# Performance work log

Measured on AMD Instinct MI355X. Metric: run time of the kernel, lower is better.

The kernel has to match this reference:

```python
import jax, jax.numpy as jnp
import numpy as np

DIM = 1024

def _circ_conv(x, key):
    # circular convolution along last dim via FFT
    D = x.shape[-1]
    return jnp.fft.irfft(jnp.fft.rfft(x, axis=-1) * jnp.fft.rfft(key), n=D, axis=-1)

def _circ_corr(x, key):
    # circular correlation: conjugate the key spectrum
    D = x.shape[-1]
    return jnp.fft.irfft(jnp.fft.rfft(x, axis=-1) * jnp.conj(jnp.fft.rfft(key)), n=D, axis=-1)

def setup_inputs() -> dict:
    key = jax.random.key(0)
    k0, k1, k2 = jax.random.split(key, 3)
    B, T, D = 4, 2048, DIM
    x = jax.random.normal(k0, (B, T, D), dtype=jnp.float32)
    bind_key = jax.random.normal(k1, (D,), dtype=jnp.float32) * 0.02
    unbind_key = jax.random.normal(k2, (D,), dtype=jnp.float32) * 0.02
    gate = jnp.ones((1,), dtype=jnp.float32)
    decay = jnp.asarray(0.9, dtype=jnp.float32)
    return {"x": x, "bind_key": bind_key, "unbind_key": unbind_key, "gate": gate, "decay": decay}

def reference(x, bind_key, unbind_key, gate, decay):
    B, T, D = x.shape
    bound = _circ_conv(x, bind_key)                      # (B, T, D)
    d = jax.nn.sigmoid(decay)
    pos = jnp.arange(T, dtype=x.dtype)
    diff = pos[:, None] - pos[None, :]                   # (T, T)
    causal = diff >= 0
    # clamp exponent to avoid inf*0 on masked (t < s) entries; math identical to tril mask
    decay_matrix = jnp.where(causal, d ** jnp.maximum(diff, 0.0), 0.0)
    hologram = jnp.einsum('ts,bsd->btd', decay_matrix, bound)
    retrieved = _circ_corr(hologram, unbind_key)
    return x + gate * retrieved
```

## Files before the change

kernel.cpp:

```cpp
#include <hip/hip_runtime.h>
#include <hip/hip_bf16.h>

constexpr int Dd = 1024;
constexpr int Tt = 2048;
constexpr int Bb = 4;
constexpr int Rr = Bb * Tt;
constexpr int NCH = 32;
constexpr int CL  = 64;
constexpr int HOR = 32;
constexpr int SCB = Bb * NCH * 2;
constexpr int CBL = 64;
constexpr int RSN = 1032;

typedef __attribute__((ext_vector_type(2))) float f32x2;
typedef __attribute__((ext_vector_type(4))) float f32x4;
typedef __attribute__((ext_vector_type(16))) float f32x16;
typedef __attribute__((ext_vector_type(8))) short bf16x8;

__device__ __forceinline__ float sigmoidf_(float v) {
    return 1.0f / (1.0f + expf(-v));
}

__device__ __forceinline__ short bf16bits(float f) {
    union { __hip_bfloat16 b; short s; } u;
    u.b = __float2bfloat16(f);
    return u.s;
}

__device__ __forceinline__ void async16(const void* g, void* l) {
    __builtin_amdgcn_global_load_lds(
        (const __attribute__((address_space(1))) unsigned int*)g,
        (__attribute__((address_space(3))) unsigned int*)l,
        16, 0, 0);
}

__global__ void k_scan(const float* __restrict__ x,
                       const float* __restrict__ bind,
                       const float* __restrict__ unbind,
                       const float* __restrict__ decay,
                       __hip_bfloat16* __restrict__ xs,
                       float* __restrict__ c) {
    __shared__ float sb[Dd];
    __shared__ float su[Dd];
    __shared__ float sp[256];

    const int tid = threadIdx.x;
    if (blockIdx.x >= CBL) {
        const int sid = blockIdx.x - CBL;
        const int dh = sid & 1;
        const int ch = (sid >> 1) & (NCH - 1);
        const int b  = sid >> 6;
        const float dd = sigmoidf_(decay[0]);
        const int t0 = ch * CL;
        const int d  = dh * 512 + tid * 2;
        f32x2 h = (f32x2){0.f, 0.f};
        if (ch != 0) {
            const size_t pb = ((size_t)b * Tt + (size_t)(t0 - HOR)) * Dd + d;
            #pragma unroll 8
            for (int t = 0; t < HOR; ++t) {
                f32x2 v = *(const f32x2*)&x[pb + (size_t)t * Dd];
                h = dd * h + v;
            }
        }
        const size_t base = ((size_t)b * Tt + (size_t)t0) * Dd + d;
        #pragma unroll 8
        for (int t = 0; t < CL; ++t) {
            f32x2 v = *(const f32x2*)&x[base + (size_t)t * Dd];
            h = dd * h + v;
            ushort2 o;
            o.x = (unsigned short)bf16bits(h[0]);
            o.y = (unsigned short)bf16bits(h[1]);
            *(ushort2*)&xs[base + (size_t)t * Dd] = o;
        }
    } else {
        for (int j = tid; j < Dd; j += 256) { sb[j] = bind[j]; su[j] = unbind[j]; }
        __syncthreads();
        const int n_loc = tid >> 4;
        const int seg = tid & 15;
        const int n = (int)blockIdx.x * 16 + n_loc;
        float acc = 0.f;
        #pragma unroll 8
        for (int i = 0; i < 64; ++i) {
            const int m = i * 16 + seg;
            acc = fmaf(su[m], sb[(m + n) & (Dd - 1)], acc);
        }
        sp[tid] = acc;
        __syncthreads();
        if (tid < 16) {
            float s = 0.f;
            #pragma unroll
            for (int j = 0; j < 16; ++j) s += sp[tid * 16 + j];
            c[(int)blockIdx.x * 16 + tid] = s;
        }
    }
}

__global__ __launch_bounds__(256, 3) void k_gemm(
    const __hip_bfloat16* __restrict__ A,
    const float* __restrict__ c,
    const float* __restrict__ x,
    const float* __restrict__ gate,
    float* __restrict__ out)
{
    __shared__ __align__(16) __hip_bfloat16 sA[128 * 64];
    __shared__ __align__(16) __hip_bfloat16 rs[8][RSN];
    __shared__ float cs[Dd];

    const int tid = threadIdx.x;
    const int wave = tid >> 6;
    const int lane = tid & 63;

    const int id  = blockIdx.x;
    const int xcd = id & 7;
    const int rr  = id >> 3;
    const int tn  = rr & 7;
    const int gg  = rr >> 3;
    const int tile_m = (xcd * 8 + gg) * 128;
    const int tile_n = tn * 128;

    #pragma unroll
    for (int j = 0; j < 4; ++j) cs[tid + j * 256] = c[tid + j * 256];
    __syncthreads();
    #pragma unroll
    for (int s = 0; s < 8; ++s)
        for (int t = tid; t < RSN; t += 256)
            rs[s][t] = __float2bfloat16(cs[(-(t + s)) & (Dd - 1)]);

    const int wm = (wave & 1) * 64;
    const int wn = (wave >> 1) * 64;

    f32x16 acc[2][2];
    #pragma unroll
    for (int i = 0; i < 2; ++i)
        #pragma unroll
        for (int j = 0; j < 2; ++j)
            #pragma unroll
            for (int e = 0; e < 16; ++e)
                acc[i][j][e] = 0.f;

    const int r8 = lane >> 3;
    const int gchunk = (lane & 7) ^ (r8 & 7);
    const int fm  = lane & 31;
    const int fsw = fm & 7;
    const int fc0 = lane >> 5;

    const int ng0 = tile_n + wn + fm;

    for (int k0 = 0; k0 < Dd; k0 += 64) {
        __syncthreads();
        #pragma unroll
        for (int j = 0; j < 4; ++j) {
            const int row = wave * 32 + j * 8;
            async16(A + (size_t)(tile_m + row + r8) * Dd + k0 + gchunk * 8,
                    &sA[row * 64]);
        }
        __syncthreads();

        #pragma unroll
        for (int kh = 0; kh < 4; ++kh) {
            const int ck = k0 + (kh * 2 + fc0) * 8;
            bf16x8 af[2], bfr[2];
            #pragma unroll
            for (int sm = 0; sm < 2; ++sm)
                af[sm] = *(const bf16x8*)
                    &sA[(wm + sm * 32 + fm) * 64 + ((kh * 2 + fc0) ^ fsw) * 8];
            #pragma unroll
            for (int sn = 0; sn < 2; ++sn) {
                const int bi = (ck - (ng0 + sn * 32)) & (Dd - 1);
                bfr[sn] = *(const bf16x8*)&rs[bi & 7][bi & ~7];
            }
            #pragma unroll
            for (int sm = 0; sm < 2; ++sm)
                #pragma unroll
                for (int sn = 0; sn < 2; ++sn)
                    acc[sm][sn] = __builtin_amdgcn_mfma_f32_32x32x16_bf16(
                        af[sm], bfr[sn], acc[sm][sn], 0, 0, 0);
        }
    }

    const float g = gate[0];
    #pragma unroll
    for (int sm = 0; sm < 2; ++sm) {
        #pragma unroll
        for (int sn = 0; sn < 2; ++sn) {
            const int colg = tile_n + wn + sn * 32 + (lane & 31);
            #pragma unroll
            for (int g1 = 0; g1 < 4; ++g1) {
                const int row0 = tile_m + wm + sm * 32 + g1 * 8 + (lane >> 5) * 4;
                #pragma unroll
                for (int r0 = 0; r0 < 4; ++r0) {
                    const size_t off = (size_t)(row0 + r0) * Dd + colg;
                    out[off] = fmaf(g, acc[sm][sn][g1 * 4 + r0], x[off]);
                }
            }
        }
    }
}

extern "C" void kernel_launch(void* const* d_in, const int* in_sizes, int n_in,
                              void* d_out, int out_size, void* d_ws, size_t ws_size,
                              hipStream_t stream) {
    const float* x      = (const float*)d_in[0];
    const float* bind   = (const float*)d_in[1];
    const float* unbind = (const float*)d_in[2];
    const float* gate   = (const float*)d_in[3];
    const float* decay  = (const float*)d_in[4];
    float* out = (float*)d_out;

    char* ws = (char*)d_ws;
    __hip_bfloat16* xs = (__hip_bfloat16*)ws;
    float* c = (float*)(ws + (size_t)Rr * Dd * 2);

    k_scan<<<dim3(SCB + CBL), dim3(256), 0, stream>>>(x, bind, unbind, decay, xs, c);
    k_gemm<<<dim3(512),       dim3(256), 0, stream>>>(xs, c, x, gate, out);
}
```

Before: 122.7 us.

## Fuse decayed scan into GEMM A-tile production with double-buffered LDS

Drops the separate scan kernel and its bf16 intermediate in global memory. The GEMM kernel now computes the decayed prefix scan for each 128x64 A tile itself: half the threads scan the next K stage into a second LDS buffer while all waves run MFMAs on the current one. Tiles grow to 128x256 with 512 threads, giving 256 blocks. This removes the intermediate write and re-read, but x is read repeatedly: each N tile redoes the scan, and each 32-row segment adds a 32-row warm-up. The scan loads are strided and sit on a serial FMA chain inside the K loop, which can stall the MFMA pipeline.

```diff
diff --git a/kernel.cpp b/kernel.cpp
--- a/kernel.cpp
+++ b/kernel.cpp
@@ -5,15 +5,13 @@
 constexpr int Tt = 2048;
 constexpr int Bb = 4;
 constexpr int Rr = Bb * Tt;
-constexpr int NCH = 32;
-constexpr int CL  = 64;
 constexpr int HOR = 32;
-constexpr int SCB = Bb * NCH * 2;
-constexpr int CBL = 64;
 constexpr int RSN = 1032;
+constexpr int BM  = 128;
+constexpr int BN  = 256;
+constexpr int BK  = 64;
+constexpr int NST = Dd / BK;
 
-typedef __attribute__((ext_vector_type(2))) float f32x2;
-typedef __attribute__((ext_vector_type(4))) float f32x4;
 typedef __attribute__((ext_vector_type(16))) float f32x16;
 typedef __attribute__((ext_vector_type(8))) short bf16x8;
 
@@ -21,88 +19,42 @@
     return 1.0f / (1.0f + expf(-v));
 }
 
-__device__ __forceinline__ short bf16bits(float f) {
-    union { __hip_bfloat16 b; short s; } u;
-    u.b = __float2bfloat16(f);
-    return u.s;
-}
-
-__device__ __forceinline__ void async16(const void* g, void* l) {
-    __builtin_amdgcn_global_load_lds(
-        (const __attribute__((address_space(1))) unsigned int*)g,
-        (__attribute__((address_space(3))) unsigned int*)l,
-        16, 0, 0);
-}
-
-__global__ void k_scan(const float* __restrict__ x,
-                       const float* __restrict__ bind,
-                       const float* __restrict__ unbind,
-                       const float* __restrict__ decay,
-                       __hip_bfloat16* __restrict__ xs,
-                       float* __restrict__ c) {
+__global__ void k_c(const float* __restrict__ bind,
+                    const float* __restrict__ unbind,
+                    float* __restrict__ c) {
     __shared__ float sb[Dd];
     __shared__ float su[Dd];
     __shared__ float sp[256];
-
     const int tid = threadIdx.x;
-    if (blockIdx.x >= CBL) {
-        const int sid = blockIdx.x - CBL;
-        const int dh = sid & 1;
-        const int ch = (sid >> 1) & (NCH - 1);
-        const int b  = sid >> 6;
-        const float dd = sigmoidf_(decay[0]);
-        const int t0 = ch * CL;
-        const int d  = dh * 512 + tid * 2;
-        f32x2 h = (f32x2){0.f, 0.f};
-        if (ch != 0) {
-            const size_t pb = ((size_t)b * Tt + (size_t)(t0 - HOR)) * Dd + d;
-            #pragma unroll 8
-            for (int t = 0; t < HOR; ++t) {
-                f32x2 v = *(const f32x2*)&x[pb + (size_t)t * Dd];
-                h = dd * h + v;
-            }
-        }
-        const size_t base = ((size_t)b * Tt + (size_t)t0) * Dd + d;
-        #pragma unroll 8
-        for (int t = 0; t < CL; ++t) {
-            f32x2 v = *(const f32x2*)&x[base + (size_t)t * Dd];
-            h = dd * h + v;
-            ushort2 o;
-            o.x = (unsigned short)bf16bits(h[0]);
-            o.y = (unsigned short)bf16bits(h[1]);
-            *(ushort2*)&xs[base + (size_t)t * Dd] = o;
-        }
-    } else {
-        for (int j = tid; j < Dd; j += 256) { sb[j] = bind[j]; su[j] = unbind[j]; }
-        __syncthreads();
-        const int n_loc = tid >> 4;
-        const int seg = tid & 15;
-        const int n = (int)blockIdx.x * 16 + n_loc;
-        float acc = 0.f;
-        #pragma unroll 8
-        for (int i = 0; i < 64; ++i) {
-            const int m = i * 16 + seg;
-            acc = fmaf(su[m], sb[(m + n) & (Dd - 1)], acc);
-        }
-        sp[tid] = acc;
-        __syncthreads();
-        if (tid < 16) {
-            float s = 0.f;
-            #pragma unroll
-            for (int j = 0; j < 16; ++j) s += sp[tid * 16 + j];
-            c[(int)blockIdx.x * 16 + tid] = s;
-        }
+    for (int j = tid; j < Dd; j += 256) { sb[j] = bind[j]; su[j] = unbind[j]; }
+    __syncthreads();
+    const int n_loc = tid >> 4;
+    const int seg = tid & 15;
+    const int n = (int)blockIdx.x * 16 + n_loc;
+    float acc = 0.f;
+    #pragma unroll 8
+    for (int i = 0; i < 64; ++i) {
+        const int m = i * 16 + seg;
+        acc = fmaf(su[m], sb[(m + n) & (Dd - 1)], acc);
+    }
+    sp[tid] = acc;
+    __syncthreads();
+    if (tid < 16) {
+        float s = 0.f;
+        #pragma unroll
+        for (int j = 0; j < 16; ++j) s += sp[tid * 16 + j];
+        c[(int)blockIdx.x * 16 + tid] = s;
     }
 }
 
-__global__ __launch_bounds__(256, 3) void k_gemm(
-    const __hip_bfloat16* __restrict__ A,
+__global__ __launch_bounds__(512) void k_fused(
+    const float* __restrict__ x,
     const float* __restrict__ c,
-    const float* __restrict__ x,
+    const float* __restrict__ decay,
     const float* __restrict__ gate,
     float* __restrict__ out)
 {
-    __shared__ __align__(16) __hip_bfloat16 sA[128 * 64];
+    __shared__ __align__(16) __hip_bfloat16 sA[2][BM * BK];
     __shared__ __align__(16) __hip_bfloat16 rs[8][RSN];
     __shared__ float cs[Dd];
 
@@ -113,21 +65,49 @@
     const int id  = blockIdx.x;
     const int xcd = id & 7;
     const int rr  = id >> 3;
-    const int tn  = rr & 7;
-    const int gg  = rr >> 3;
-    const int tile_m = (xcd * 8 + gg) * 128;
-    const int tile_n = tn * 128;
+    const int im  = xcd * 8 + (rr >> 2);
+    const int in_ = rr & 3;
+    const int tile_m = im * BM;
+    const int tile_n = in_ * BN;
+    const int chunk  = im & 15;
 
-    #pragma unroll
-    for (int j = 0; j < 4; ++j) cs[tid + j * 256] = c[tid + j * 256];
+    const float dd = sigmoidf_(decay[0]);
+
+    cs[tid] = c[tid];
+    cs[tid + 512] = c[tid + 512];
     __syncthreads();
     #pragma unroll
     for (int s = 0; s < 8; ++s)
-        for (int t = tid; t < RSN; t += 256)
+        for (int t = tid; t < RSN; t += 512)
             rs[s][t] = __float2bfloat16(cs[(-(t + s)) & (Dd - 1)]);
 
-    const int wm = (wave & 1) * 64;
-    const int wn = (wave >> 1) * 64;
+    const int scol = tid & 63;
+    const int seg  = tid >> 6;
+    auto scan = [&](int bb, int k0) {
+        const int nw = (chunk == 0 && seg == 0) ? 0 : HOR;
+        const float* xp = x + (size_t)(tile_m + seg * 32 - nw) * Dd + (k0 + scol);
+        float h = 0.f;
+        if (nw) {
+            #pragma unroll 8
+            for (int i = 0; i < HOR; ++i)
+                h = dd * h + xp[(size_t)i * Dd];
+            xp += (size_t)HOR * Dd;
+        }
+        #pragma unroll 8
+        for (int i = 0; i < 32; ++i) {
+            h = dd * h + xp[(size_t)i * Dd];
+            const int rl = seg * 32 + i;
+            sA[bb][rl * 64 + ((((scol >> 3) ^ (rl & 7)) * 8) + (scol & 7))] =
+                __float2bfloat16(h);
+        }
+    };
+
+    const int wm  = (wave & 1) * 64;
+    const int wn  = (wave >> 1) * 64;
+    const int fm  = lane & 31;
+    const int fsw = fm & 7;
+    const int fc0 = lane >> 5;
+    const int ng0 = tile_n + wn + fm;
 
     f32x16 acc[2][2];
     #pragma unroll
@@ -138,32 +118,22 @@
             for (int e = 0; e < 16; ++e)
                 acc[i][j][e] = 0.f;
 
-    const int r8 = lane >> 3;
-    const int gchunk = (lane & 7) ^ (r8 & 7);
-    const int fm  = lane & 31;
-    const int fsw = fm & 7;
-    const int fc0 = lane >> 5;
+    if (tid < 256) scan(0, 0);
+    __syncthreads();
 
-    const int ng0 = tile_n + wn + fm;
-
-    for (int k0 = 0; k0 < Dd; k0 += 64) {
-        __syncthreads();
-        #pragma unroll
-        for (int j = 0; j < 4; ++j) {
-            const int row = wave * 32 + j * 8;
-            async16(A + (size_t)(tile_m + row + r8) * Dd + k0 + gchunk * 8,
-                    &sA[row * 64]);
-        }
-        __syncthreads();
-
+    for (int s = 0; s < NST; ++s) {
+        const int bb = s & 1;
+        if (tid < 256 && s + 1 < NST) scan(bb ^ 1, (s + 1) * BK);
+        const int k0 = s * BK;
         #pragma unroll
         for (int kh = 0; kh < 4; ++kh) {
-            const int ck = k0 + (kh * 2 + fc0) * 8;
+            const int kc = kh * 2 + fc0;
+            const int ck = k0 + kc * 8;
             bf16x8 af[2], bfr[2];
             #pragma unroll
             for (int sm = 0; sm < 2; ++sm)
                 af[sm] = *(const bf16x8*)
-                    &sA[(wm + sm * 32 + fm) * 64 + ((kh * 2 + fc0) ^ fsw) * 8];
+                    &sA[bb][(wm + sm * 32 + fm) * 64 + (kc ^ fsw) * 8];
             #pragma unroll
             for (int sn = 0; sn < 2; ++sn) {
                 const int bi = (ck - (ng0 + sn * 32)) & (Dd - 1);
@@ -176,6 +146,7 @@
                     acc[sm][sn] = __builtin_amdgcn_mfma_f32_32x32x16_bf16(
                         af[sm], bfr[sn], acc[sm][sn], 0, 0, 0);
         }
+        __syncthreads();
     }
 
     const float g = gate[0];
@@ -207,10 +178,8 @@
     const float* decay  = (const float*)d_in[4];
     float* out = (float*)d_out;
 
-    char* ws = (char*)d_ws;
-    __hip_bfloat16* xs = (__hip_bfloat16*)ws;
-    float* c = (float*)(ws + (size_t)Rr * Dd * 2);
+    float* c = (float*)d_ws;
 
-    k_scan<<<dim3(SCB + CBL), dim3(256), 0, stream>>>(x, bind, unbind, decay, xs, c);
-    k_gemm<<<dim3(512),       dim3(256), 0, stream>>>(xs, c, x, gate, out);
+    k_c    <<<dim3(64),  dim3(256), 0, stream>>>(bind, unbind, c);
+    k_fused<<<dim3(256), dim3(512), 0, stream>>>(x, c, decay, gate, out);
 }
```

After: 165.5 us. +34.9%, slower.
